# Performance work log

Measured on AMD Instinct MI355X. Metric: run time of the kernel, lower is better.

Reference implementation:

```python
import jax, jax.numpy as jnp
import numpy as np

K = 16  # kNN neighbors


def _knn(xb, k):
    # xb: [N, H] -> [N, k] nearest-neighbor indices (self excluded)
    sq = jnp.sum(xb * xb, axis=-1)
    d = sq[:, None] + sq[None, :] - 2.0 * (xb @ xb.T)  # squared distances [N, N]
    n = xb.shape[0]
    big = jnp.asarray(1e30, d.dtype)
    d = d + jnp.eye(n, dtype=d.dtype) * big  # mask self-loops
    _, idx = jax.lax.top_k(-d, k)
    return idx


def _edgeconv(h, W0, b0, W1, b1, k):
    # Dynamic kNN graph on current features + EdgeConv with 2-layer MLP, aggr='add'
    idx = jax.vmap(lambda xb: _knn(xb, k))(h)                 # [B, N, k]
    xj = jax.vmap(lambda xb, ib: xb[ib])(h, idx)              # [B, N, k, H] gather neighbors
    xi = jnp.broadcast_to(h[:, :, None, :], xj.shape)         # [B, N, k, H]
    m = jnp.concatenate([xi, xj - xi], axis=-1)               # [B, N, k, 2H]
    e = jax.nn.elu(m @ W0 + b0)
    e = jax.nn.elu(e @ W1 + b1)
    return jnp.sum(e, axis=2)                                 # 'add' aggregation over neighbors


def _forward(x, W_in0, b_in0, W_in1, b_in1, W_in2, b_in2,
             W_e0, b_e0, W_e1, b_e1,
             W_o0, b_o0, W_o1, b_o1, W_o2, b_o2):
    # input network (in_layers=3)
    h = jax.nn.elu(x @ W_in0 + b_in0)
    h = jax.nn.elu(h @ W_in1 + b_in1)
    h = jax.nn.elu(h @ W_in2 + b_in2)
    # agg_layers=2 blocks of dynamic-kNN EdgeConv
    for l in range(W_e0.shape[0]):
        h = _edgeconv(h, W_e0[l], b_e0[l], W_e1[l], b_e1[l], K)
    # global max pool over nodes of each graph (pool='max')
    g = jnp.max(h, axis=1)                                    # [B, H]
    # output network (out_layers=3)
    g = jax.nn.elu(g @ W_o0 + b_o0)
    g = jax.nn.elu(g @ W_o1 + b_o1)
    logits = g @ W_o2 + b_o2
    return jax.nn.log_softmax(logits, axis=1)


def setup_inputs() -> dict:
    key = jax.random.key(0)
    ks = jax.random.split(key, 8)
    B, N, F, H, C, A = 128, 512, 5, 64, 10, 2
    s = jnp.float32(0.1)

    def w(k, shape):
        return jax.random.normal(k, shape, jnp.float32) * s

    return {
        'x': jax.random.normal(ks[0], (B, N, F), jnp.float32),
        'W_in0': w(ks[1], (F, H)), 'b_in0': jnp.zeros((H,), jnp.float32),
        'W_in1': w(ks[2], (H, H)), 'b_in1': jnp.zeros((H,), jnp.float32),
        'W_in2': w(ks[3], (H, H)), 'b_in2': jnp.zeros((H,), jnp.float32),
        'W_e0': w(ks[4], (A, 2 * H, H)), 'b_e0': jnp.zeros((A, H), jnp.float32),
        'W_e1': w(ks[5], (A, H, H)), 'b_e1': jnp.zeros((A, H), jnp.float32),
        'W_o0': w(ks[6], (H, H)), 'b_o0': jnp.zeros((H,), jnp.float32),
        'W_o1': w(ks[7], (H, H)), 'b_o1': jnp.zeros((H,), jnp.float32),
        'W_o2': w(jax.random.fold_in(key, 99), (H, C)), 'b_o2': jnp.zeros((C,), jnp.float32),
    }


def reference(x, W_in0, b_in0, W_in1, b_in1, W_in2, b_in2,
              W_e0, b_e0, W_e1, b_e1,
              W_o0, b_o0, W_o1, b_o1, W_o2, b_o2):
    return _forward(x, W_in0, b_in0, W_in1, b_in1, W_in2, b_in2,
                    W_e0, b_e0, W_e1, b_e1,
                    W_o0, b_o0, W_o1, b_o1, W_o2, b_o2)
```

## Files before the change

kernel.cpp:

```cpp
#include <hip/hip_runtime.h>
#include <hip/hip_fp16.h>
#include <cmath>

typedef _Float16 f16;
typedef _Float16 f16x8 __attribute__((ext_vector_type(8)));
typedef float f32x4 __attribute__((ext_vector_type(4)));

#define B_ 128
#define N_ 512
#define H_ 64
#define K_ 16

__device__ __forceinline__ float elu_(float x) { return x > 0.f ? x : (__expf(x) - 1.f); }
__device__ __forceinline__ unsigned umin_(unsigned a, unsigned b) { return a < b ? a : b; }
__device__ __forceinline__ unsigned umax_(unsigned a, unsigned b) { return a > b ? a : b; }
__device__ __forceinline__ f32x4 mfma16(f16x8 a, f16x8 b, f32x4 c) {
    return __builtin_amdgcn_mfma_f32_16x16x32_f16(a, b, c, 0, 0, 0);
}
__device__ __forceinline__ f32x4 splat4(float v) { f32x4 r; r[0]=v; r[1]=v; r[2]=v; r[3]=v; return r; }
__device__ __forceinline__ unsigned mbcnt_(unsigned long long mask) {
    return __builtin_amdgcn_mbcnt_hi((unsigned)(mask >> 32),
           __builtin_amdgcn_mbcnt_lo((unsigned)mask, 0u));
}
__device__ __forceinline__ f16 hexp_(f16 x) {
    __half h = *(__half*)&x; h = hexp(h); return *(f16*)&h;
}
__device__ __forceinline__ f16x8 elu8h_(f16x8 x) {
    f16x8 z; f16x8 one;
    #pragma unroll
    for (int i = 0; i < 8; ++i) { z[i] = (f16)0.f; one[i] = (f16)1.f; }
    f16x8 mx = __builtin_elementwise_max(x, z);
    f16x8 mn = __builtin_elementwise_min(x, z);
    f16x8 e;
    #pragma unroll
    for (int i = 0; i < 8; ++i) e[i] = hexp_(mn[i]);
    return mx + e - one;
}
__device__ __forceinline__ unsigned wmax64_(unsigned v) {
    v = umax_(v, (unsigned)__builtin_amdgcn_update_dpp(0, (int)v, 0x111, 0xf, 0xf, true));
    v = umax_(v, (unsigned)__builtin_amdgcn_update_dpp(0, (int)v, 0x112, 0xf, 0xf, true));
    v = umax_(v, (unsigned)__builtin_amdgcn_update_dpp(0, (int)v, 0x114, 0xf, 0xf, true));
    v = umax_(v, (unsigned)__builtin_amdgcn_update_dpp(0, (int)v, 0x118, 0xf, 0xf, true));
    v = umax_(v, (unsigned)__builtin_amdgcn_update_dpp(0, (int)v, 0x142, 0xa, 0xf, true));
    v = umax_(v, (unsigned)__builtin_amdgcn_update_dpp(0, (int)v, 0x143, 0xc, 0xf, true));
    return (unsigned)__builtin_amdgcn_readlane((int)v, 63);
}
__device__ __forceinline__ float rsum16lo_(float x) {
    x += __int_as_float(__builtin_amdgcn_update_dpp(0, __float_as_int(x), 0x101, 0xf, 0xf, true));
    x += __int_as_float(__builtin_amdgcn_update_dpp(0, __float_as_int(x), 0x102, 0xf, 0xf, true));
    x += __int_as_float(__builtin_amdgcn_update_dpp(0, __float_as_int(x), 0x104, 0xf, 0xf, true));
    x += __int_as_float(__builtin_amdgcn_update_dpp(0, __float_as_int(x), 0x108, 0xf, 0xf, true));
    return x;
}

__global__ __launch_bounds__(256) void prep_kernel(const float* __restrict__ We0,
        const float* __restrict__ We1,
        f16* __restrict__ PW, f16* __restrict__ QW, f16* __restrict__ W1T)
{
    const int t = threadIdx.x;
    #pragma unroll
    for (int l = 0; l < 2; ++l) {
        const float* A  = We0 + l*8192;
        const float* B1 = We1 + l*4096;
        for (int i = t; i < 4096; i += 256) {
            const int n = i >> 6, k = i & 63;
            const float wa = A[k*64 + n];
            const float wb = A[(k+64)*64 + n];
            PW [l*4096 + n*64 + k] = (f16)(wa - wb);
            QW [l*4096 + n*64 + k] = (f16)wb;
            W1T[l*4096 + n*64 + k] = (f16)B1[k*64 + n];
        }
    }
}

__global__ __launch_bounds__(256) void mlp_kernel(const float* __restrict__ x,
        const float* __restrict__ W0, const float* __restrict__ b0,
        const float* __restrict__ W1, const float* __restrict__ b1,
        const float* __restrict__ W2, const float* __restrict__ b2,
        f16* __restrict__ hout, float* __restrict__ sqout)
{
    __shared__ f16 tile[4][16*72];
    __shared__ f16 w1t[64*80];
    __shared__ f16 w2t[64*80];
    const int tid = threadIdx.x;
    const int lane = tid & 63, wid = tid >> 6;
    const int m = lane & 15, q = lane >> 4;
    const int rowbase = blockIdx.x*64 + wid*16;
    f16* tw = tile[wid];

    {
        const int k  = tid >> 2;
        const int n0 = (tid & 3) << 4;
        #pragma unroll
        for (int jj = 0; jj < 4; ++jj) {
            const float4 v1 = *(const float4*)(W1 + k*64 + n0 + jj*4);
            const float4 v2 = *(const float4*)(W2 + k*64 + n0 + jj*4);
            const int nb = n0 + jj*4;
            w1t[(nb+0)*80 + k] = (f16)v1.x; w1t[(nb+1)*80 + k] = (f16)v1.y;
            w1t[(nb+2)*80 + k] = (f16)v1.z; w1t[(nb+3)*80 + k] = (f16)v1.w;
            w2t[(nb+0)*80 + k] = (f16)v2.x; w2t[(nb+1)*80 + k] = (f16)v2.y;
            w2t[(nb+2)*80 + k] = (f16)v2.z; w2t[(nb+3)*80 + k] = (f16)v2.w;
        }
    }

    f16x8 af0, af1;
    {
        const float* xp = x + (size_t)(rowbase + m)*5;
        #pragma unroll
        for (int jj = 0; jj < 8; ++jj) { int k = q*8+jj; af0[jj] = (k < 5) ? (f16)xp[k] : (f16)0.f; }
    }
    f32x4 acc[4];
    #pragma unroll
    for (int t = 0; t < 4; ++t) {
        f16x8 bf;
        #pragma unroll
        for (int jj = 0; jj < 8; ++jj) { int k = q*8+jj; bf[jj] = (k < 5) ? (f16)W0[k*64 + t*16+m] : (f16)0.f; }
        acc[t] = splat4(b0[t*16+m]);
        acc[t] = mfma16(af0, bf, acc[t]);
    }
    #pragma unroll
    for (int t = 0; t < 4; ++t)
        #pragma unroll
        for (int r = 0; r < 4; ++r)
            tw[(q*4+r)*72 + t*16+m] = (f16)elu_(acc[t][r]);
    af0 = *(const f16x8*)(tw + m*72 + q*8);
    af1 = *(const f16x8*)(tw + m*72 + q*8 + 32);
    __syncthreads();

    #pragma unroll
    for (int t = 0; t < 4; ++t) {
        f16x8 bfa = *(const f16x8*)(w1t + (t*16+m)*80 + q*8);
        f16x8 bfb = *(const f16x8*)(w1t + (t*16+m)*80 + q*8 + 32);
        acc[t] = splat4(b1[t*16+m]);
        acc[t] = mfma16(af0, bfa, acc[t]);
        acc[t] = mfma16(af1, bfb, acc[t]);
    }
    #pragma unroll
    for (int t = 0; t < 4; ++t)
        #pragma unroll
        for (int r = 0; r < 4; ++r)
            tw[(q*4+r)*72 + t*16+m] = (f16)elu_(acc[t][r]);
    af0 = *(const f16x8*)(tw + m*72 + q*8);
    af1 = *(const f16x8*)(tw + m*72 + q*8 + 32);

    #pragma unroll
    for (int t = 0; t < 4; ++t) {
        f16x8 bfa = *(const f16x8*)(w2t + (t*16+m)*80 + q*8);
        f16x8 bfb = *(const f16x8*)(w2t + (t*16+m)*80 + q*8 + 32);
        acc[t] = splat4(b2[t*16+m]);
        acc[t] = mfma16(af0, bfa, acc[t]);
        acc[t] = mfma16(af1, bfb, acc[t]);
    }
    float s[4] = {0.f,0.f,0.f,0.f};
    #pragma unroll
    for (int t = 0; t < 4; ++t)
        #pragma unroll
        for (int r = 0; r < 4; ++r) {
            float v = elu_(acc[t][r]);
            hout[(size_t)(rowbase + q*4 + r)*64 + t*16 + m] = (f16)v;
            s[r] += v*v;
        }
    #pragma unroll
    for (int r = 0; r < 4; ++r) s[r] = rsum16lo_(s[r]);
    if (m == 0) {
        #pragma unroll
        for (int r = 0; r < 4; ++r) sqout[rowbase + q*4 + r] = s[r];
    }
}

__global__ __launch_bounds__(512, 8) void knn_kernel(const f16* __restrict__ hin,
        const float* __restrict__ sq, int* __restrict__ idxout,
        const f16* __restrict__ PWl, const float* __restrict__ be,
        const f16* __restrict__ QWl,
        f16* __restrict__ Pout, f16* __restrict__ Qout)
{
    __shared__ unsigned keys[16*512];
    const int lane = threadIdx.x & 63;
    const int wid  = threadIdx.x >> 6;
    const int m = lane & 15, q = lane >> 4;
    const int bid = ((blockIdx.x & 7) << 9) | (blockIdx.x >> 3);
    const int b  = bid >> 5;
    const int rt = bid & 31;
    const int rowbase = rt*16;
    const f16* hb = hin + (size_t)b*N_*H_;
    const float* sqb = sq + b*N_;

    f16x8 af0, af1;
    {
        const f16* Ap = hb + (size_t)(rowbase + m)*64 + q*8;
        af0 = *(const f16x8*)Ap;
        af1 = *(const f16x8*)(Ap + 32);
    }
    const int colb0 = wid*16;
    f16x8 bf0[4], bf1[4];
    float sc[4];
    #pragma unroll
    for (int cti = 0; cti < 4; ++cti) {
        const f16* Bp = hb + (size_t)(colb0 + cti*128 + m)*64 + q*8;
        bf0[cti] = *(const f16x8*)Bp;
        bf1[cti] = *(const f16x8*)(Bp + 32);
        sc[cti] = sqb[colb0 + cti*128 + m];
    }
    int base_r[4];
    #pragma unroll
    for (int r = 0; r < 4; ++r) {
        const int row = q*4 + r;
        base_r[r] = row*512 + ((colb0 + m) ^ (row << 1));
    }
    #pragma unroll
    for (int cti = 0; cti < 4; ++cti) {
        f32x4 acc = splat4(0.f);
        acc = mfma16(af0, bf0[cti], acc);
        acc = mfma16(af1, bf1[cti], acc);
        #pragma unroll
        for (int r = 0; r < 4; ++r) {
            float d = fmaf(-2.f, acc[r], sc[cti]);
            unsigned u = __float_as_uint(d);
            u ^= (0x80000000u | (unsigned)((int)u >> 31));
            unsigned key = (u & 0xFFFFFE00u) | (unsigned)(colb0 + cti*128 + m);
            keys[base_r[r] + cti*128] = key;
        }
    }
    __syncthreads();

    unsigned kk[2][8];
    #pragma unroll
    for (int rr = 0; rr < 2; ++rr) {
        const int ri = wid*2 + rr;
        *(uint4*)&kk[rr][0] = *(const uint4*)(keys + ri*512 + lane*4);
        *(uint4*)&kk[rr][4] = *(const uint4*)(keys + ri*512 + 256 + lane*4);
    }
    unsigned* scr = keys + wid*2*512;

    unsigned v[2];
    #pragma unroll
    for (int rr = 0; rr < 2; ++rr) {
        unsigned mn = kk[rr][0];
        #pragma unroll
        for (int s2 = 1; s2 < 8; ++s2) mn = umin_(mn, kk[rr][s2]);
        v[rr] = mn;
    }
    unsigned T[2] = {0u,0u};
    #pragma unroll
    for (int bit = 31; bit >= 9; --bit) {
        #pragma unroll
        for (int rr = 0; rr < 2; ++rr) {
            unsigned cand = T[rr] | (1u << bit);
            int c = __popcll(__ballot(v[rr] < cand));
            T[rr] = (c < 17) ? cand : T[rr];
        }
    }
    T[0] |= 511u; T[1] |= 511u;

    unsigned cnt[2];
    #pragma unroll
    for (int rr = 0; rr < 2; ++rr) {
        unsigned long long bal[8];
        #pragma unroll
        for (int s2 = 0; s2 < 8; ++s2) bal[s2] = __ballot(kk[rr][s2] <= T[rr]);
        unsigned base = 0;
        #pragma unroll
        for (int s2 = 0; s2 < 8; ++s2) {
            if (kk[rr][s2] <= T[rr]) {
                unsigned pos = base + mbcnt_(bal[s2]);
                if (pos < 64u) scr[rr*64 + pos] = kk[rr][s2];
            }
            base += (unsigned)__popcll(bal[s2]);
        }
        cnt[rr] = base;
    }

    #pragma unroll
    for (int rr = 0; rr < 2; ++rr) {
        const unsigned cc_ = umin_(cnt[rr], 64u);
        const int ri = wid*2 + rr;
        const unsigned rowglob = (unsigned)(rowbase + ri);
        bool act = lane < (int)cc_;
        unsigned mv = act ? scr[rr*64 + lane] : 0u;
        if (act && (mv & 511u) == rowglob) { act = false; mv = 0u; }
        int e = __popcll(__ballot(act)) - 16;
        while (e > 0) {
            unsigned mx = wmax64_(mv);
            if (mv == mx) { act = false; mv = 0u; }
            --e;
        }
        int* outp = idxout + ((size_t)b*N_ + rowglob)*K_;
        unsigned long long bal = __ballot(act);
        unsigned rank = mbcnt_(bal);
        if (act) outp[rank] = (int)(mv & 511u);
    }

    {
        const int t = wid & 3;
        const int n = t*16 + m;
        f32x4 acc = (wid < 4) ? splat4(be[n]) : splat4(0.f);
        const f16* Wp = (wid < 4) ? PWl : QWl;
        #pragma unroll
        for (int cc = 0; cc < 2; ++cc) {
            const f16x8 afc = cc ? af1 : af0;
            const f16x8 bb = *(const f16x8*)(Wp + n*64 + cc*32 + q*8);
            acc = mfma16(afc, bb, acc);
        }
        f16* outp = (wid < 4) ? Pout : Qout;
        #pragma unroll
        for (int r = 0; r < 4; ++r)
            outp[((size_t)b*N_ + rowbase + q*4 + r)*64 + t*16 + m] = (f16)acc[r];
    }
}

__device__ __forceinline__ void edge_node_(size_t r0, f16x8 pa, f16x8 pb,
        f16x8 qa, f16x8 qb, const f16x8 (&bf)[2][4], const float (&bcol)[4],
        f16* __restrict__ out, float* __restrict__ sqout, int lane)
{
    f16x8 af0 = elu8h_(pa + qa);
    f16x8 af1 = elu8h_(pb + qb);
    f32x4 acc[4];
    #pragma unroll
    for (int t = 0; t < 4; ++t) acc[t] = splat4(bcol[t]);
    #pragma unroll
    for (int t = 0; t < 4; ++t) acc[t] = mfma16(af0, bf[0][t], acc[t]);
    #pragma unroll
    for (int t = 0; t < 4; ++t) acc[t] = mfma16(af1, bf[1][t], acc[t]);
    float ssum = 0.f;
    #pragma unroll
    for (int t = 0; t < 4; ++t) {
        float s = elu_(acc[t][0]) + elu_(acc[t][1]) + elu_(acc[t][2]) + elu_(acc[t][3]);
        s += __shfl_xor(s, 16);
        s += __shfl_xor(s, 32);
        if (lane < 16) out[r0*64 + t*16 + lane] = (f16)s;
        ssum += s*s;
    }
    ssum = rsum16lo_(ssum);
    if (lane == 0) sqout[r0] = ssum;
}

__global__ __launch_bounds__(256, 4) void edge_kernel(const f16* __restrict__ P,
        const f16* __restrict__ Q, const int* __restrict__ idx,
        const f16* __restrict__ W1T, const float* __restrict__ b1,
        f16* __restrict__ out, float* __restrict__ sqout)
{
    const int lane = threadIdx.x & 63;
    const int wid  = threadIdx.x >> 6;
    const int m = lane & 15, q = lane >> 4;

    f16x8 bf[2][4];
    #pragma unroll
    for (int cc = 0; cc < 2; ++cc)
        #pragma unroll
        for (int t = 0; t < 4; ++t)
            bf[cc][t] = *(const f16x8*)(W1T + (t*16 + m)*64 + cc*32 + q*8);
    float bcol[4];
    #pragma unroll
    for (int t = 0; t < 4; ++t) bcol[t] = b1[t*16 + m];

    const int bid = ((blockIdx.x & 7) << 9) | (blockIdx.x >> 3);
    const int node0 = bid*16 + wid*4;
    const int gbase = node0 & ~(N_-1);
    const int c0a = q*8, c0b = q*8 + 32;
    int jv[4];
    #pragma unroll
    for (int i = 0; i < 4; ++i) jv[i] = idx[(size_t)(node0 + i)*K_ + m];

    f16x8 pA[4], pB[4], qA[4], qB[4];
    #pragma unroll
    for (int k2 = 0; k2 < 4; ++k2) {
        const size_t r0 = (size_t)(node0 + k2);
        const size_t g0 = (size_t)(gbase + jv[k2]);
        pA[k2] = *(const f16x8*)(P + r0*64 + c0a);
        pB[k2] = *(const f16x8*)(P + r0*64 + c0b);
        qA[k2] = *(const f16x8*)(Q + g0*64 + c0a);
        qB[k2] = *(const f16x8*)(Q + g0*64 + c0b);
    }
    #pragma unroll
    for (int k2 = 0; k2 < 4; ++k2)
        edge_node_((size_t)(node0 + k2), pA[k2], pB[k2], qA[k2], qB[k2],
                   bf, bcol, out, sqout, lane);
}

__global__ __launch_bounds__(512) void final_kernel(const f16* __restrict__ hin,
        const float* __restrict__ Wo0, const float* __restrict__ bo0,
        const float* __restrict__ Wo1, const float* __restrict__ bo1,
        const float* __restrict__ Wo2, const float* __restrict__ bo2,
        float* __restrict__ out)
{
    __shared__ float smax[64][64];
    __shared__ float g0[64], g1[64], g2[64], part[8][64], lg[10];
    const int t = threadIdx.x;
    const int b = blockIdx.x;
    const int cg = t & 7, rg = t >> 3;

    float mx[8];
    #pragma unroll
    for (int e = 0; e < 8; ++e) mx[e] = -3.0e38f;
    #pragma unroll
    for (int i = 0; i < 8; ++i) {
        const int row = rg + i*64;
        f16x8 vv = *(const f16x8*)(hin + ((size_t)b*N_ + row)*64 + cg*8);
        #pragma unroll
        for (int e = 0; e < 8; ++e) mx[e] = fmaxf(mx[e], (float)vv[e]);
    }
    #pragma unroll
    for (int e = 0; e < 8; ++e) smax[rg][cg*8 + e] = mx[e];
    __syncthreads();
    for (int s = 32; s >= 1; s >>= 1) {
        if (rg < s) {
            #pragma unroll
            for (int e = 0; e < 8; ++e)
                smax[rg][cg*8+e] = fmaxf(smax[rg][cg*8+e], smax[rg+s][cg*8+e]);
        }
        __syncthreads();
    }
    if (t < 64) g0[t] = smax[0][t];
    __syncthreads();

    const int j = t & 63, p = t >> 6;
    {
        float a = 0.f;
        #pragma unroll
        for (int c = 0; c < 8; ++c) a += g0[p*8 + c]*Wo0[(p*8 + c)*64 + j];
        part[p][j] = a;
    }
    __syncthreads();
    if (t < 64) {
        float a = bo0[t];
        #pragma unroll
        for (int p2 = 0; p2 < 8; ++p2) a += part[p2][t];
        g1[t] = elu_(a);
    }
    __syncthreads();
    {
        float a = 0.f;
        #pragma unroll
        for (int c = 0; c < 8; ++c) a += g1[p*8 + c]*Wo1[(p*8 + c)*64 + j];
        part[p][j] = a;
    }
    __syncthreads();
    if (t < 64) {
        float a = bo1[t];
        #pragma unroll
        for (int p2 = 0; p2 < 8; ++p2) a += part[p2][t];
        g2[t] = elu_(a);
    }
    __syncthreads();
    if (t < 10) { float a = bo2[t]; for (int c = 0; c < 64; ++c) a += g2[c]*Wo2[c*10 + t]; lg[t] = a; }
    __syncthreads();
    if (t == 0) {
        float mxl = lg[0];
        for (int i = 1; i < 10; ++i) mxl = fmaxf(mxl, lg[i]);
        float s = 0.f;
        for (int i = 0; i < 10; ++i) s += expf(lg[i] - mxl);
        const float lse = mxl + logf(s);
        for (int i = 0; i < 10; ++i) out[b*10 + i] = lg[i] - lse;
    }
}

extern "C" void kernel_launch(void* const* d_in, const int* in_sizes, int n_in,
                              void* d_out, int out_size, void* d_ws, size_t ws_size,
                              hipStream_t stream) {
    const float* x     = (const float*)d_in[0];
    const float* W_in0 = (const float*)d_in[1];
    const float* b_in0 = (const float*)d_in[2];
    const float* W_in1 = (const float*)d_in[3];
    const float* b_in1 = (const float*)d_in[4];
    const float* W_in2 = (const float*)d_in[5];
    const float* b_in2 = (const float*)d_in[6];
    const float* W_e0  = (const float*)d_in[7];
    const float* b_e0  = (const float*)d_in[8];
    const float* W_e1  = (const float*)d_in[9];
    const float* b_e1  = (const float*)d_in[10];
    const float* Wo0   = (const float*)d_in[11];
    const float* bo0   = (const float*)d_in[12];
    const float* Wo1   = (const float*)d_in[13];
    const float* bo1   = (const float*)d_in[14];
    const float* Wo2   = (const float*)d_in[15];
    const float* bo2   = (const float*)d_in[16];

    char* ws = (char*)d_ws;
    f16*    hA   = (f16*)(ws);
    f16*    hB   = (f16*)(ws + 8388608);
    f16*    Pb   = (f16*)(ws + 16777216);
    f16*    Qb   = (f16*)(ws + 25165824);
    int*    idxb = (int*)(ws + 33554432);
    float*  sqb  = (float*)(ws + 37748736);
    f16*    PW   = (f16*)(ws + 38010880);
    f16*    QW   = (f16*)(ws + 38027264);
    f16*    W1T  = (f16*)(ws + 38043648);

    prep_kernel<<<1, 256, 0, stream>>>(W_e0, W_e1, PW, QW, W1T);
    mlp_kernel<<<1024, 256, 0, stream>>>(x, W_in0, b_in0, W_in1, b_in1, W_in2, b_in2,
                                         hA, sqb);
    knn_kernel<<<4096, 512, 0, stream>>>(hA, sqb, idxb, PW, b_e0, QW, Pb, Qb);
    edge_kernel<<<4096, 256, 0, stream>>>(Pb, Qb, idxb, W1T, b_e1, hB, sqb);
    knn_kernel<<<4096, 512, 0, stream>>>(hB, sqb, idxb, PW + 4096, b_e0 + 64, QW + 4096, Pb, Qb);
    edge_kernel<<<4096, 256, 0, stream>>>(Pb, Qb, idxb, W1T + 4096, b_e1 + 64, hA, sqb);

    final_kernel<<<128, 512, 0, stream>>>(hA, Wo0, bo0, Wo1, bo1, Wo2, bo2, (float*)d_out);
}
```

Baseline: 303.2 us.

## Fuse weight prep into MLP kernel and replace iterative max removal with radix select

The separate single-block weight-prep kernel is removed and its work spread over the first 128 blocks of the input MLP kernel, saving a launch and a serialized tiny kernel. In the kNN kernel, final top-16 selection among up to 64 candidates no longer repeatedly finds and removes the wave-wide maximum. It now runs a 32-step bitwise radix search for the 17th-smallest key using ballot/popcount for both rows at once. This gives a fixed instruction count in place of a data-dependent loop of DPP reductions, but relies on keys being unique so that exactly 16 fall below the threshold.

Result: faster. 293.2 us (-3.3%).

```diff
diff --git a/kernel.cpp b/kernel.cpp
--- a/kernel.cpp
+++ b/kernel.cpp
@@ -35,15 +35,6 @@
     #pragma unroll
     for (int i = 0; i < 8; ++i) e[i] = hexp_(mn[i]);
     return mx + e - one;
-}
-__device__ __forceinline__ unsigned wmax64_(unsigned v) {
-    v = umax_(v, (unsigned)__builtin_amdgcn_update_dpp(0, (int)v, 0x111, 0xf, 0xf, true));
-    v = umax_(v, (unsigned)__builtin_amdgcn_update_dpp(0, (int)v, 0x112, 0xf, 0xf, true));
-    v = umax_(v, (unsigned)__builtin_amdgcn_update_dpp(0, (int)v, 0x114, 0xf, 0xf, true));
-    v = umax_(v, (unsigned)__builtin_amdgcn_update_dpp(0, (int)v, 0x118, 0xf, 0xf, true));
-    v = umax_(v, (unsigned)__builtin_amdgcn_update_dpp(0, (int)v, 0x142, 0xa, 0xf, true));
-    v = umax_(v, (unsigned)__builtin_amdgcn_update_dpp(0, (int)v, 0x143, 0xc, 0xf, true));
-    return (unsigned)__builtin_amdgcn_readlane((int)v, 63);
 }
 __device__ __forceinline__ float rsum16lo_(float x) {
     x += __int_as_float(__builtin_amdgcn_update_dpp(0, __float_as_int(x), 0x101, 0xf, 0xf, true));
@@ -53,30 +44,12 @@
     return x;
 }
 
-__global__ __launch_bounds__(256) void prep_kernel(const float* __restrict__ We0,
-        const float* __restrict__ We1,
-        f16* __restrict__ PW, f16* __restrict__ QW, f16* __restrict__ W1T)
-{
-    const int t = threadIdx.x;
-    #pragma unroll
-    for (int l = 0; l < 2; ++l) {
-        const float* A  = We0 + l*8192;
-        const float* B1 = We1 + l*4096;
-        for (int i = t; i < 4096; i += 256) {
-            const int n = i >> 6, k = i & 63;
-            const float wa = A[k*64 + n];
-            const float wb = A[(k+64)*64 + n];
-            PW [l*4096 + n*64 + k] = (f16)(wa - wb);
-            QW [l*4096 + n*64 + k] = (f16)wb;
-            W1T[l*4096 + n*64 + k] = (f16)B1[k*64 + n];
-        }
-    }
-}
-
 __global__ __launch_bounds__(256) void mlp_kernel(const float* __restrict__ x,
         const float* __restrict__ W0, const float* __restrict__ b0,
         const float* __restrict__ W1, const float* __restrict__ b1,
         const float* __restrict__ W2, const float* __restrict__ b2,
+        const float* __restrict__ We0, const float* __restrict__ We1,
+        f16* __restrict__ PW, f16* __restrict__ QW, f16* __restrict__ W1T,
         f16* __restrict__ hout, float* __restrict__ sqout)
 {
     __shared__ f16 tile[4][16*72];
@@ -87,6 +60,18 @@
     const int m = lane & 15, q = lane >> 4;
     const int rowbase = blockIdx.x*64 + wid*16;
     f16* tw = tile[wid];
+
+    if (blockIdx.x < 128 && tid < 64) {
+        const int l = blockIdx.x >> 6, k = blockIdx.x & 63;
+        const float* A  = We0 + l*8192;
+        const float* B1 = We1 + l*4096;
+        const float wa = A[k*64 + tid];
+        const float wb = A[(k+64)*64 + tid];
+        const float w1 = B1[k*64 + tid];
+        PW [l*4096 + tid*64 + k] = (f16)(wa - wb);
+        QW [l*4096 + tid*64 + k] = (f16)wb;
+        W1T[l*4096 + tid*64 + k] = (f16)w1;
+    }
 
     {
         const int k  = tid >> 2;
@@ -270,24 +255,33 @@
         cnt[rr] = base;
     }
 
+    unsigned mv[2];
     #pragma unroll
     for (int rr = 0; rr < 2; ++rr) {
         const unsigned cc_ = umin_(cnt[rr], 64u);
-        const int ri = wid*2 + rr;
-        const unsigned rowglob = (unsigned)(rowbase + ri);
-        bool act = lane < (int)cc_;
-        unsigned mv = act ? scr[rr*64 + lane] : 0u;
-        if (act && (mv & 511u) == rowglob) { act = false; mv = 0u; }
-        int e = __popcll(__ballot(act)) - 16;
-        while (e > 0) {
-            unsigned mx = wmax64_(mv);
-            if (mv == mx) { act = false; mv = 0u; }
-            --e;
-        }
+        const unsigned rowglob = (unsigned)(rowbase + wid*2 + rr);
+        unsigned v2 = (lane < (int)cc_) ? scr[rr*64 + lane] : 0xFFFFFFFFu;
+        if ((v2 & 511u) == rowglob) v2 = 0xFFFFFFFFu;
+        mv[rr] = v2;
+    }
+    unsigned Tx[2] = {0u, 0u};
+    #pragma unroll
+    for (int bit = 31; bit >= 0; --bit) {
+        #pragma unroll
+        for (int rr = 0; rr < 2; ++rr) {
+            unsigned cand = Tx[rr] | (1u << bit);
+            int c = __popcll(__ballot(mv[rr] < cand));
+            Tx[rr] = (c < 17) ? cand : Tx[rr];
+        }
+    }
+    #pragma unroll
+    for (int rr = 0; rr < 2; ++rr) {
+        const unsigned rowglob = (unsigned)(rowbase + wid*2 + rr);
         int* outp = idxout + ((size_t)b*N_ + rowglob)*K_;
-        unsigned long long bal = __ballot(act);
+        const bool sel = mv[rr] < Tx[rr];
+        unsigned long long bal = __ballot(sel);
         unsigned rank = mbcnt_(bal);
-        if (act) outp[rank] = (int)(mv & 511u);
+        if (sel) outp[rank] = (int)(mv[rr] & 511u);
     }
 
     {
@@ -486,9 +480,8 @@
     f16*    QW   = (f16*)(ws + 38027264);
     f16*    W1T  = (f16*)(ws + 38043648);
 
-    prep_kernel<<<1, 256, 0, stream>>>(W_e0, W_e1, PW, QW, W1T);
     mlp_kernel<<<1024, 256, 0, stream>>>(x, W_in0, b_in0, W_in1, b_in1, W_in2, b_in2,
-                                         hA, sqb);
+                                         W_e0, W_e1, PW, QW, W1T, hA, sqb);
     knn_kernel<<<4096, 512, 0, stream>>>(hA, sqb, idxb, PW, b_e0, QW, Pb, Qb);
     edge_kernel<<<4096, 256, 0, stream>>>(Pb, Qb, idxb, W1T, b_e1, hB, sqb);
     knn_kernel<<<4096, 512, 0, stream>>>(hB, sqb, idxb, PW + 4096, b_e0 + 64, QW + 4096, Pb, Qb);
```

## Fold weight prep into MLP kernel and use radix-4 threshold search in kNN

Applied to the files above, without the earlier changes.

Removes the single-block prep_kernel launch and spreads the edge-weight transpose/convert across the first 128 blocks of mlp_kernel, which saves one serialized launch. In knn_kernel, the bitwise binary search for the 16th-smallest key threshold now resolves two bits per step using three ballots. This halves the number of dependent steps but adds more ballots per step. The combined edit mixes launch-overhead reduction with a latency-oriented selection rewrite.

Result: faster. 293.4 us (-3.2%).

```diff
diff --git a/kernel.cpp b/kernel.cpp
--- a/kernel.cpp
+++ b/kernel.cpp
@@ -53,30 +53,12 @@
     return x;
 }
 
-__global__ __launch_bounds__(256) void prep_kernel(const float* __restrict__ We0,
-        const float* __restrict__ We1,
-        f16* __restrict__ PW, f16* __restrict__ QW, f16* __restrict__ W1T)
-{
-    const int t = threadIdx.x;
-    #pragma unroll
-    for (int l = 0; l < 2; ++l) {
-        const float* A  = We0 + l*8192;
-        const float* B1 = We1 + l*4096;
-        for (int i = t; i < 4096; i += 256) {
-            const int n = i >> 6, k = i & 63;
-            const float wa = A[k*64 + n];
-            const float wb = A[(k+64)*64 + n];
-            PW [l*4096 + n*64 + k] = (f16)(wa - wb);
-            QW [l*4096 + n*64 + k] = (f16)wb;
-            W1T[l*4096 + n*64 + k] = (f16)B1[k*64 + n];
-        }
-    }
-}
-
 __global__ __launch_bounds__(256) void mlp_kernel(const float* __restrict__ x,
         const float* __restrict__ W0, const float* __restrict__ b0,
         const float* __restrict__ W1, const float* __restrict__ b1,
         const float* __restrict__ W2, const float* __restrict__ b2,
+        const float* __restrict__ We0, const float* __restrict__ We1,
+        f16* __restrict__ PW, f16* __restrict__ QW, f16* __restrict__ W1T,
         f16* __restrict__ hout, float* __restrict__ sqout)
 {
     __shared__ f16 tile[4][16*72];
@@ -87,6 +69,18 @@
     const int m = lane & 15, q = lane >> 4;
     const int rowbase = blockIdx.x*64 + wid*16;
     f16* tw = tile[wid];
+
+    if (blockIdx.x < 128 && tid < 64) {
+        const int l = blockIdx.x >> 6, k = blockIdx.x & 63;
+        const float* A  = We0 + l*8192;
+        const float* B1 = We1 + l*4096;
+        const float wa = A[k*64 + tid];
+        const float wb = A[(k+64)*64 + tid];
+        const float w1 = B1[k*64 + tid];
+        PW [l*4096 + tid*64 + k] = (f16)(wa - wb);
+        QW [l*4096 + tid*64 + k] = (f16)wb;
+        W1T[l*4096 + tid*64 + k] = (f16)w1;
+    }
 
     {
         const int k  = tid >> 2;
@@ -242,13 +236,24 @@
     }
     unsigned T[2] = {0u,0u};
     #pragma unroll
-    for (int bit = 31; bit >= 9; --bit) {
+    for (int p = 30; p >= 10; p -= 2) {
         #pragma unroll
         for (int rr = 0; rr < 2; ++rr) {
-            unsigned cand = T[rr] | (1u << bit);
-            int c = __popcll(__ballot(v[rr] < cand));
-            T[rr] = (c < 17) ? cand : T[rr];
-        }
+            const unsigned c1 = T[rr] | (1u << p);
+            const unsigned c2 = T[rr] | (2u << p);
+            const unsigned c3 = T[rr] | (3u << p);
+            const int n1 = __popcll(__ballot(v[rr] < c1));
+            const int n2 = __popcll(__ballot(v[rr] < c2));
+            const int n3 = __popcll(__ballot(v[rr] < c3));
+            const unsigned d = (n3 < 17) ? 3u : (n2 < 17) ? 2u : (n1 < 17) ? 1u : 0u;
+            T[rr] |= d << p;
+        }
+    }
+    #pragma unroll
+    for (int rr = 0; rr < 2; ++rr) {
+        const unsigned cand = T[rr] | (1u << 9);
+        const int c = __popcll(__ballot(v[rr] < cand));
+        if (c < 17) T[rr] = cand;
     }
     T[0] |= 511u; T[1] |= 511u;
 
@@ -486,9 +491,8 @@
     f16*    QW   = (f16*)(ws + 38027264);
     f16*    W1T  = (f16*)(ws + 38043648);
 
-    prep_kernel<<<1, 256, 0, stream>>>(W_e0, W_e1, PW, QW, W1T);
     mlp_kernel<<<1024, 256, 0, stream>>>(x, W_in0, b_in0, W_in1, b_in1, W_in2, b_in2,
-                                         hA, sqb);
+                                         W_e0, W_e1, PW, QW, W1T, hA, sqb);
     knn_kernel<<<4096, 512, 0, stream>>>(hA, sqb, idxb, PW, b_e0, QW, Pb, Qb);
     edge_kernel<<<4096, 256, 0, stream>>>(Pb, Qb, idxb, W1T, b_e1, hB, sqb);
     knn_kernel<<<4096, 512, 0, stream>>>(hB, sqb, idxb, PW + 4096, b_e0 + 64, QW + 4096, Pb, Qb);
```
